# Performance work log

Measured on AMD Instinct MI355X. Metric: run time of the kernel, lower is better.

The kernel has to match this reference:

```python
import jax, jax.numpy as jnp
import numpy as np

B = 8192          # batch of sequences (original module used 1; math broadcasts)
T = 99            # sequential FastGRNN steps
D_IN = 32         # per-step input features (3168 = 99 * 32)
D_H = 100         # hidden size
R_W, R_U = 16, 25 # low ranks
N_CLS = 6


def setup_inputs() -> dict:
    key = jax.random.key(0)
    ks = jax.random.split(key, 11)
    s = 0.1
    return {
        "x": jax.random.normal(ks[0], (B, T * D_IN), dtype=jnp.float32),
        "W1": jax.random.normal(ks[1], (D_IN, R_W), dtype=jnp.float32) * s,
        "W2": jax.random.normal(ks[2], (R_W, D_H), dtype=jnp.float32) * s,
        "U1": jax.random.normal(ks[3], (D_H, R_U), dtype=jnp.float32) * s,
        "U2": jax.random.normal(ks[4], (R_U, D_H), dtype=jnp.float32) * s,
        "bias_gate": jax.random.normal(ks[5], (1, D_H), dtype=jnp.float32) * s,
        "bias_update": jax.random.normal(ks[6], (1, D_H), dtype=jnp.float32) * s,
        "zeta": jax.random.normal(ks[7], (1, 1), dtype=jnp.float32),
        "nu": jax.random.normal(ks[8], (1, 1), dtype=jnp.float32),
        "FC": jax.random.normal(ks[9], (D_H, N_CLS), dtype=jnp.float32) * s,
        "FCbias": jax.random.normal(ks[10], (1, N_CLS), dtype=jnp.float32) * s,
    }


def reference(x, W1, W2, U1, U2, bias_gate, bias_update, zeta, nu, FC, FCbias):
    b = x.shape[0]
    # x[:, 32*i:32*(i+1)] for i in 0..T-1  ->  [T, B, D_IN] for scan
    xs = x.reshape(b, T, D_IN).transpose(1, 0, 2)
    sz = jax.nn.sigmoid(zeta)  # [1,1]
    sn = jax.nn.sigmoid(nu)    # [1,1]
    H0 = jnp.zeros((b, D_H), dtype=x.dtype)

    def step(H, XX):
        # low-rank projections: (XX @ W1) @ W2 + (H @ U1) @ U2
        c = (XX @ W1) @ W2 + (H @ U1) @ U2          # [B, D_H]
        g = jax.nn.sigmoid(c + bias_gate)
        h = jnp.tanh(c + bias_update)
        # exact blend from source: tanh branch is NOT scaled by (1-g)
        H_new = g * H + (sz * (1.0 - g) + sn * h)
        return H_new, None

    H, _ = jax.lax.scan(step, H0, xs)
    score = H @ FC + FCbias                          # [B, N_CLS]
    return score
```

## Files before the change

### kernel.cpp

```cpp
#include <hip/hip_runtime.h>
#include <math.h>


typedef __attribute__((ext_vector_type(8))) short short8_t;
typedef __attribute__((ext_vector_type(4))) float f32x4;

#define TSTEPS 99
#define DIN    32
#define DH     100
#define XROW   3168
#define NCLS   6
#define LOG2E  1.44269504088896340736f

#define NFRAG  70
#define OFF_EG (NFRAG * 256)
#define OFF_EU (OFF_EG + 128)
#define OFF_SZ (OFF_EU + 128)
#define OFF_SN (OFF_SZ + 1)

__device__ __forceinline__ unsigned cvtpk(float a, float b) {
    unsigned r;
    asm("v_cvt_pk_bf16_f32 %0, %1, %2" : "=v"(r) : "v"(a), "v"(b));
    return r;
}
__device__ __forceinline__ float fbits(unsigned u) { return __int_as_float((int)u); }

union F8 { unsigned u4[4]; short8_t s8; };

__global__ __launch_bounds__(256) void precomp(
    const float* __restrict__ W1, const float* __restrict__ W2,
    const float* __restrict__ U1, const float* __restrict__ U2,
    const float* __restrict__ bg, const float* __restrict__ bu,
    const float* __restrict__ zeta, const float* __restrict__ nu,
    float* __restrict__ ws)
{
    const int i = blockIdx.x * 256 + threadIdx.x;
    if (i < NFRAG * 64 / 2 * 2) {
        if (i < NFRAG / 2 * 64) {}
    }
    if (i < 2240) {
        const int lane = i & 63, f = i >> 6;
        const int jt = f / 5, kt = f % 5;
        const int u = lane & 15, g4 = lane >> 4;
        const int col = jt * 16 + u;
        float v[8];
        #pragma unroll
        for (int e = 0; e < 8; ++e) {
            float s = 0.f;
            if (col < DH) {
                if (kt < 4) {
                    const int k = kt * 32 + g4 * 8 + e;
                    if (k < DH) {
                        #pragma unroll
                        for (int r = 0; r < 25; ++r)
                            s = fmaf(U1[k * 25 + r], U2[r * DH + col], s);
                    }
                } else {
                    const int k = g4 * 8 + e;
                    #pragma unroll
                    for (int r = 0; r < 16; ++r)
                        s = fmaf(W1[k * 16 + r], W2[r * DH + col], s);
                }
            }
            v[e] = s * LOG2E;
        }
        unsigned hi[4], lo[4];
        #pragma unroll
        for (int rr = 0; rr < 4; ++rr) {
            const float a = v[2 * rr], b = v[2 * rr + 1];
            const unsigned ph = cvtpk(a, b);
            hi[rr] = ph;
            lo[rr] = cvtpk(a - fbits(ph << 16), b - fbits(ph & 0xffff0000u));
        }
        uint4* B = (uint4*)ws;
        B[(f * 2 + 0) * 64 + lane] = make_uint4(hi[0], hi[1], hi[2], hi[3]);
        B[(f * 2 + 1) * 64 + lane] = make_uint4(lo[0], lo[1], lo[2], lo[3]);
    } else if (i < 2240 + 128) {
        const int p = i - 2240;
        ws[OFF_EG + p] = (p < DH) ? expf(-bg[p]) : 1.f;
    } else if (i < 2240 + 256) {
        const int p = i - 2240 - 128;
        ws[OFF_EU + p] = (p < DH) ? expf(-2.f * bu[p]) : 1.f;
    } else if (i == 2240 + 256) {
        ws[OFF_SZ] = 1.f / (1.f + expf(-zeta[0]));
    } else if (i == 2240 + 257) {
        ws[OFF_SN] = 1.f / (1.f + expf(-nu[0]));
    }
}

__global__ __launch_bounds__(256, 1) void fastgrnn_main(
    const float* __restrict__ x, const float* __restrict__ ws,
    const float* __restrict__ FC, const float* __restrict__ FCbias,
    float* __restrict__ out)
{
    __shared__ float Hl[2][2][128][18];

    const int tid  = threadIdx.x;
    const int lane = tid & 63;
    const int ww   = __builtin_amdgcn_readfirstlane(tid >> 6);
    const int rg   = ww >> 1;
    const int jhalf = ww & 1;
    const int jbase = jhalf * 4;
    const int jn    = jhalf ? 3 : 4;
    const int u  = lane & 15;
    const int g4 = lane >> 4;
    const int rowbase = blockIdx.x * 32 + rg * 16;

    for (int z = tid; z < 2 * 2 * 128 * 18; z += 256) ((float*)Hl)[z] = 0.f;

    F8 Breg[4][5][2];
    #pragma unroll
    for (int jt = 0; jt < 4; ++jt) {
        if (jt < jn) {
            #pragma unroll
            for (int kt = 0; kt < 5; ++kt) {
                #pragma unroll
                for (int s = 0; s < 2; ++s) {
                    const int F = ((jbase + jt) * 5 + kt) * 2 + s;
                    Breg[jt][kt][s].s8 =
                        *(const short8_t*)((const uint4*)ws + F * 64 + lane);
                    asm volatile("" : "+v"(Breg[jt][kt][s].u4[0]),
                                      "+v"(Breg[jt][kt][s].u4[1]),
                                      "+v"(Breg[jt][kt][s].u4[2]),
                                      "+v"(Breg[jt][kt][s].u4[3]));
                }
            }
        }
    }
    float eg_r[4], eu_r[4];
    #pragma unroll
    for (int jt = 0; jt < 4; ++jt) {
        const int unit = (jbase + jt) * 16 + u;
        eg_r[jt] = ws[OFF_EG + unit];
        eu_r[jt] = ws[OFF_EU + unit];
        asm volatile("" : "+v"(eg_r[jt]), "+v"(eu_r[jt]));
    }
    const float sz = ws[OFF_SZ];
    const float sn = ws[OFF_SN];

    const float* __restrict__ xrow = x + (size_t)(rowbase + u) * XROW;

    const f32x4 zero4 = {0.f, 0.f, 0.f, 0.f};
    f32x4 Hold[4];
    #pragma unroll
    for (int jt = 0; jt < 4; ++jt) Hold[jt] = zero4;

    __syncthreads();

    for (int t = 0; t < TSTEPS; ++t) {
        const int rb = t & 1, wb = rb ^ 1;

        F8 xhi, xlo;
        #pragma unroll
        for (int r = 0; r < 4; ++r) {
            const float2 xv = *(const float2*)(xrow + t * DIN + g4 * 8 + 2 * r);
            const unsigned ph = cvtpk(xv.x, xv.y);
            xhi.u4[r] = ph;
            xlo.u4[r] = cvtpk(xv.x - fbits(ph << 16),
                              xv.y - fbits(ph & 0xffff0000u));
        }

        F8 ahi[4], alo[4];
        #pragma unroll
        for (int kt = 0; kt < 4; ++kt) {
            #pragma unroll
            for (int r = 0; r < 4; ++r) {
                const int k = kt * 32 + g4 * 8 + 2 * r;
                const float h0 = Hl[rg][rb][k][u];
                const float h1 = Hl[rg][rb][k + 1][u];
                const unsigned ph = cvtpk(h0, h1);
                ahi[kt].u4[r] = ph;
                alo[kt].u4[r] = cvtpk(h0 - fbits(ph << 16),
                                      h1 - fbits(ph & 0xffff0000u));
            }
        }

        f32x4 acc[4];
        #pragma unroll
        for (int jt = 0; jt < 4; ++jt) acc[jt] = zero4;

        #pragma unroll
        for (int kt = 0; kt < 5; ++kt) {
            const short8_t Ah = (kt < 4) ? ahi[kt].s8 : xhi.s8;
            const short8_t Al = (kt < 4) ? alo[kt].s8 : xlo.s8;
            #pragma unroll
            for (int jt = 0; jt < 4; ++jt)
                if (jt < jn)
                    acc[jt] = __builtin_amdgcn_mfma_f32_16x16x32_bf16(
                        Al, Breg[jt][kt][1].s8, acc[jt], 0, 0, 0);
            #pragma unroll
            for (int jt = 0; jt < 4; ++jt)
                if (jt < jn)
                    acc[jt] = __builtin_amdgcn_mfma_f32_16x16x32_bf16(
                        Al, Breg[jt][kt][0].s8, acc[jt], 0, 0, 0);
            #pragma unroll
            for (int jt = 0; jt < 4; ++jt)
                if (jt < jn)
                    acc[jt] = __builtin_amdgcn_mfma_f32_16x16x32_bf16(
                        Ah, Breg[jt][kt][1].s8, acc[jt], 0, 0, 0);
            #pragma unroll
            for (int jt = 0; jt < 4; ++jt)
                if (jt < jn)
                    acc[jt] = __builtin_amdgcn_mfma_f32_16x16x32_bf16(
                        Ah, Breg[jt][kt][0].s8, acc[jt], 0, 0, 0);
        }

        #pragma unroll
        for (int jt = 0; jt < 4; ++jt) {
            if (jt < jn) {
                f32x4 hn;
                #pragma unroll
                for (int i = 0; i < 4; ++i) {
                    const float cc = acc[jt][i];
                    const float E  = __builtin_amdgcn_exp2f(-cc);
                    const float g  = __builtin_amdgcn_rcpf(fmaf(E, eg_r[jt], 1.f));
                    float p = E * E * eu_r[jt];
                    p = fminf(p, 1e30f);
                    const float h = (1.f - p) * __builtin_amdgcn_rcpf(1.f + p);
                    hn[i] = fmaf(g, Hold[jt][i], fmaf(sn, h, fmaf(-sz, g, sz)));
                }
                Hold[jt] = hn;
                const int unit = (jbase + jt) * 16 + u;
                float* dst = &Hl[rg][wb][unit][g4 * 4];
                *(float2*)(dst)     = make_float2(hn[0], hn[1]);
                *(float2*)(dst + 2) = make_float2(hn[2], hn[3]);
            }
        }
        __syncthreads();
    }

    const int fb = TSTEPS & 1;
    if (tid < 192) {
        const int rl = tid / NCLS, c = tid % NCLS;
        const int erg = rl >> 4, row = rl & 15;
        float s = FCbias[c];
        for (int k = 0; k < DH; ++k)
            s = fmaf(Hl[erg][fb][k][row], FC[k * NCLS + c], s);
        out[(size_t)(blockIdx.x * 32 + rl) * NCLS + c] = s;
    }
}

extern "C" void kernel_launch(void* const* d_in, const int* in_sizes, int n_in,
                              void* d_out, int out_size, void* d_ws, size_t ws_size,
                              hipStream_t stream)
{
    const float* x    = (const float*)d_in[0];
    const float* W1   = (const float*)d_in[1];
    const float* W2   = (const float*)d_in[2];
    const float* U1   = (const float*)d_in[3];
    const float* U2   = (const float*)d_in[4];
    const float* bg   = (const float*)d_in[5];
    const float* bu   = (const float*)d_in[6];
    const float* zeta = (const float*)d_in[7];
    const float* nu   = (const float*)d_in[8];
    const float* FC   = (const float*)d_in[9];
    const float* FCb  = (const float*)d_in[10];
    float* ws  = (float*)d_ws;
    float* out = (float*)d_out;

    precomp<<<(2240 + 258 + 255) / 256, 256, 0, stream>>>(
        W1, W2, U1, U2, bg, bu, zeta, nu, ws);
    fastgrnn_main<<<256, 256, 0, stream>>>(x, ws, FC, FCb, out);
}
```

Before: 356.0 us.

## Split each block to 16 rows across 4 waves, drop lo*lo MFMA, vectorize LDS

Each block now handles 16 batch rows instead of 32, and its four waves split the seven output column tiles two per wave instead of two row groups each covering half the columns. The grid doubles to 512 blocks with launch bounds allowing two blocks per CU, so more independent recurrences run at once and each wave does less serial work per step. The lo×lo correction MFMA term is dropped, leaving three MFMAs per tile, which cuts per-step matrix work at a small precision cost. The hidden-state LDS layout is transposed so each step's reads are 16-byte vector loads, and x is loaded with float4 loads; writes become scalar stores.

```diff
diff --git a/kernel.cpp b/kernel.cpp
--- a/kernel.cpp
+++ b/kernel.cpp
@@ -35,9 +35,6 @@
     float* __restrict__ ws)
 {
     const int i = blockIdx.x * 256 + threadIdx.x;
-    if (i < NFRAG * 64 / 2 * 2) {
-        if (i < NFRAG / 2 * 64) {}
-    }
     if (i < 2240) {
         const int lane = i & 63, f = i >> 6;
         const int jt = f / 5, kt = f % 5;
@@ -88,62 +85,58 @@
     }
 }
 
-__global__ __launch_bounds__(256, 1) void fastgrnn_main(
+__global__ __launch_bounds__(256, 2) void fastgrnn_main(
     const float* __restrict__ x, const float* __restrict__ ws,
     const float* __restrict__ FC, const float* __restrict__ FCbias,
     float* __restrict__ out)
 {
-    __shared__ float Hl[2][2][128][18];
+    __shared__ __align__(16) float Hl[2][16][132];
 
     const int tid  = threadIdx.x;
     const int lane = tid & 63;
     const int ww   = __builtin_amdgcn_readfirstlane(tid >> 6);
-    const int rg   = ww >> 1;
-    const int jhalf = ww & 1;
-    const int jbase = jhalf * 4;
-    const int jn    = jhalf ? 3 : 4;
-    const int u  = lane & 15;
-    const int g4 = lane >> 4;
-    const int rowbase = blockIdx.x * 32 + rg * 16;
-
-    for (int z = tid; z < 2 * 2 * 128 * 18; z += 256) ((float*)Hl)[z] = 0.f;
-
-    F8 Breg[4][5][2];
+    const int jn   = (ww == 3) ? 1 : 2;
+    const int u    = lane & 15;
+    const int g4   = lane >> 4;
+    const int rowbase = blockIdx.x * 16;
+
+    for (int z = tid; z < 2 * 16 * 132; z += 256) ((float*)Hl)[z] = 0.f;
+
+    F8 Breg[2][5][2];
     #pragma unroll
-    for (int jt = 0; jt < 4; ++jt) {
-        if (jt < jn) {
-            #pragma unroll
-            for (int kt = 0; kt < 5; ++kt) {
-                #pragma unroll
-                for (int s = 0; s < 2; ++s) {
-                    const int F = ((jbase + jt) * 5 + kt) * 2 + s;
-                    Breg[jt][kt][s].s8 =
-                        *(const short8_t*)((const uint4*)ws + F * 64 + lane);
-                    asm volatile("" : "+v"(Breg[jt][kt][s].u4[0]),
-                                      "+v"(Breg[jt][kt][s].u4[1]),
-                                      "+v"(Breg[jt][kt][s].u4[2]),
-                                      "+v"(Breg[jt][kt][s].u4[3]));
-                }
-            }
-        }
-    }
-    float eg_r[4], eu_r[4];
+    for (int jj = 0; jj < 2; ++jj) {
+        const int jt = (2 * ww + jj > 6) ? 6 : 2 * ww + jj;
+        #pragma unroll
+        for (int kt = 0; kt < 5; ++kt) {
+            #pragma unroll
+            for (int s = 0; s < 2; ++s) {
+                const int F = (jt * 5 + kt) * 2 + s;
+                Breg[jj][kt][s].s8 =
+                    *(const short8_t*)((const uint4*)ws + F * 64 + lane);
+                asm volatile("" : "+v"(Breg[jj][kt][s].u4[0]),
+                                  "+v"(Breg[jj][kt][s].u4[1]),
+                                  "+v"(Breg[jj][kt][s].u4[2]),
+                                  "+v"(Breg[jj][kt][s].u4[3]));
+            }
+        }
+    }
+    float eg_r[2], eu_r[2];
     #pragma unroll
-    for (int jt = 0; jt < 4; ++jt) {
-        const int unit = (jbase + jt) * 16 + u;
-        eg_r[jt] = ws[OFF_EG + unit];
-        eu_r[jt] = ws[OFF_EU + unit];
-        asm volatile("" : "+v"(eg_r[jt]), "+v"(eu_r[jt]));
+    for (int jj = 0; jj < 2; ++jj) {
+        const int jt = (2 * ww + jj > 6) ? 6 : 2 * ww + jj;
+        const int unit = jt * 16 + u;
+        eg_r[jj] = ws[OFF_EG + unit];
+        eu_r[jj] = ws[OFF_EU + unit];
+        asm volatile("" : "+v"(eg_r[jj]), "+v"(eu_r[jj]));
     }
     const float sz = ws[OFF_SZ];
     const float sn = ws[OFF_SN];
 
-    const float* __restrict__ xrow = x + (size_t)(rowbase + u) * XROW;
+    const float* __restrict__ xrow = x + (size_t)(rowbase + u) * XROW + g4 * 8;
 
     const f32x4 zero4 = {0.f, 0.f, 0.f, 0.f};
-    f32x4 Hold[4];
-    #pragma unroll
-    for (int jt = 0; jt < 4; ++jt) Hold[jt] = zero4;
+    f32x4 Hold[2];
+    Hold[0] = zero4; Hold[1] = zero4;
 
     __syncthreads();
 
@@ -151,92 +144,90 @@
         const int rb = t & 1, wb = rb ^ 1;
 
         F8 xhi, xlo;
-        #pragma unroll
-        for (int r = 0; r < 4; ++r) {
-            const float2 xv = *(const float2*)(xrow + t * DIN + g4 * 8 + 2 * r);
-            const unsigned ph = cvtpk(xv.x, xv.y);
-            xhi.u4[r] = ph;
-            xlo.u4[r] = cvtpk(xv.x - fbits(ph << 16),
-                              xv.y - fbits(ph & 0xffff0000u));
+        {
+            const f32x4 xa = *(const f32x4*)(xrow + t * DIN);
+            const f32x4 xb = *(const f32x4*)(xrow + t * DIN + 4);
+            const float xs[8] = { xa.x, xa.y, xa.z, xa.w, xb.x, xb.y, xb.z, xb.w };
+            #pragma unroll
+            for (int r = 0; r < 4; ++r) {
+                const unsigned ph = cvtpk(xs[2*r], xs[2*r+1]);
+                xhi.u4[r] = ph;
+                xlo.u4[r] = cvtpk(xs[2*r]   - fbits(ph << 16),
+                                  xs[2*r+1] - fbits(ph & 0xffff0000u));
+            }
         }
 
         F8 ahi[4], alo[4];
         #pragma unroll
         for (int kt = 0; kt < 4; ++kt) {
+            const f32x4 h0 = *(const f32x4*)&Hl[rb][u][kt * 32 + g4 * 8];
+            const f32x4 h1 = *(const f32x4*)&Hl[rb][u][kt * 32 + g4 * 8 + 4];
+            const float hs[8] = { h0.x, h0.y, h0.z, h0.w, h1.x, h1.y, h1.z, h1.w };
             #pragma unroll
             for (int r = 0; r < 4; ++r) {
-                const int k = kt * 32 + g4 * 8 + 2 * r;
-                const float h0 = Hl[rg][rb][k][u];
-                const float h1 = Hl[rg][rb][k + 1][u];
-                const unsigned ph = cvtpk(h0, h1);
+                const unsigned ph = cvtpk(hs[2*r], hs[2*r+1]);
                 ahi[kt].u4[r] = ph;
-                alo[kt].u4[r] = cvtpk(h0 - fbits(ph << 16),
-                                      h1 - fbits(ph & 0xffff0000u));
-            }
-        }
-
-        f32x4 acc[4];
-        #pragma unroll
-        for (int jt = 0; jt < 4; ++jt) acc[jt] = zero4;
+                alo[kt].u4[r] = cvtpk(hs[2*r]   - fbits(ph << 16),
+                                      hs[2*r+1] - fbits(ph & 0xffff0000u));
+            }
+        }
+
+        f32x4 acc[2];
+        acc[0] = zero4; acc[1] = zero4;
 
         #pragma unroll
         for (int kt = 0; kt < 5; ++kt) {
             const short8_t Ah = (kt < 4) ? ahi[kt].s8 : xhi.s8;
             const short8_t Al = (kt < 4) ? alo[kt].s8 : xlo.s8;
             #pragma unroll
-            for (int jt = 0; jt < 4; ++jt)
-                if (jt < jn)
-                    acc[jt] = __builtin_amdgcn_mfma_f32_16x16x32_bf16(
-                        Al, Breg[jt][kt][1].s8, acc[jt], 0, 0, 0);
-            #pragma unroll
-            for (int jt = 0; jt < 4; ++jt)
-                if (jt < jn)
-                    acc[jt] = __builtin_amdgcn_mfma_f32_16x16x32_bf16(
-                        Al, Breg[jt][kt][0].s8, acc[jt], 0, 0, 0);
-            #pragma unroll
-            for (int jt = 0; jt < 4; ++jt)
-                if (jt < jn)
-                    acc[jt] = __builtin_amdgcn_mfma_f32_16x16x32_bf16(
-                        Ah, Breg[jt][kt][1].s8, acc[jt], 0, 0, 0);
-            #pragma unroll
-            for (int jt = 0; jt < 4; ++jt)
-                if (jt < jn)
-                    acc[jt] = __builtin_amdgcn_mfma_f32_16x16x32_bf16(
-                        Ah, Breg[jt][kt][0].s8, acc[jt], 0, 0, 0);
-        }
-
-        #pragma unroll
-        for (int jt = 0; jt < 4; ++jt) {
-            if (jt < jn) {
+            for (int jj = 0; jj < 2; ++jj)
+                if (jj < jn)
+                    acc[jj] = __builtin_amdgcn_mfma_f32_16x16x32_bf16(
+                        Al, Breg[jj][kt][0].s8, acc[jj], 0, 0, 0);
+            #pragma unroll
+            for (int jj = 0; jj < 2; ++jj)
+                if (jj < jn)
+                    acc[jj] = __builtin_amdgcn_mfma_f32_16x16x32_bf16(
+                        Ah, Breg[jj][kt][1].s8, acc[jj], 0, 0, 0);
+            #pragma unroll
+            for (int jj = 0; jj < 2; ++jj)
+                if (jj < jn)
+                    acc[jj] = __builtin_amdgcn_mfma_f32_16x16x32_bf16(
+                        Ah, Breg[jj][kt][0].s8, acc[jj], 0, 0, 0);
+        }
+
+        #pragma unroll
+        for (int jj = 0; jj < 2; ++jj) {
+            if (jj < jn) {
                 f32x4 hn;
                 #pragma unroll
                 for (int i = 0; i < 4; ++i) {
-                    const float cc = acc[jt][i];
+                    const float cc = acc[jj][i];
                     const float E  = __builtin_amdgcn_exp2f(-cc);
-                    const float g  = __builtin_amdgcn_rcpf(fmaf(E, eg_r[jt], 1.f));
-                    float p = E * E * eu_r[jt];
+                    const float g  = __builtin_amdgcn_rcpf(fmaf(E, eg_r[jj], 1.f));
+                    float p = E * E * eu_r[jj];
                     p = fminf(p, 1e30f);
                     const float h = (1.f - p) * __builtin_amdgcn_rcpf(1.f + p);
-                    hn[i] = fmaf(g, Hold[jt][i], fmaf(sn, h, fmaf(-sz, g, sz)));
+                    hn[i] = fmaf(g, Hold[jj][i], fmaf(sn, h, fmaf(-sz, g, sz)));
                 }
-                Hold[jt] = hn;
-                const int unit = (jbase + jt) * 16 + u;
-                float* dst = &Hl[rg][wb][unit][g4 * 4];
-                *(float2*)(dst)     = make_float2(hn[0], hn[1]);
-                *(float2*)(dst + 2) = make_float2(hn[2], hn[3]);
+                Hold[jj] = hn;
+                const int unit = (2 * ww + jj) * 16 + u;
+                Hl[wb][g4 * 4 + 0][unit] = hn[0];
+                Hl[wb][g4 * 4 + 1][unit] = hn[1];
+                Hl[wb][g4 * 4 + 2][unit] = hn[2];
+                Hl[wb][g4 * 4 + 3][unit] = hn[3];
             }
         }
         __syncthreads();
     }
 
     const int fb = TSTEPS & 1;
-    if (tid < 192) {
+    if (tid < 16 * NCLS) {
         const int rl = tid / NCLS, c = tid % NCLS;
-        const int erg = rl >> 4, row = rl & 15;
         float s = FCbias[c];
         for (int k = 0; k < DH; ++k)
-            s = fmaf(Hl[erg][fb][k][row], FC[k * NCLS + c], s);
-        out[(size_t)(blockIdx.x * 32 + rl) * NCLS + c] = s;
+            s = fmaf(Hl[fb][rl][k], FC[k * NCLS + c], s);
+        out[(size_t)(rowbase + rl) * NCLS + c] = s;
     }
 }
 
@@ -260,5 +251,5 @@
 
     precomp<<<(2240 + 258 + 255) / 256, 256, 0, stream>>>(
         W1, W2, U1, U2, bg, bu, zeta, nu, ws);
-    fastgrnn_main<<<256, 256, 0, stream>>>(x, ws, FC, FCb, out);
-}
+    fastgrnn_main<<<512, 256, 0, stream>>>(x, ws, FC, FCb, out);
+}
```

After: 311.1 us. 12.6% less time.
